# Kernel optimization log

Hardware: AMD Instinct MI355X
Metric: run time of the kernel (lower is better)

Reference implementation:

```python
import jax, jax.numpy as jnp
import numpy as np

N_NODES = 100000
N_EDGES = 1600000
N_GRAPHS = 512


def gcn_conv(x, src, dst, W, b, n_nodes):
    """PyG GCNConv: add self-loops, symmetric norm, linear, scatter-add, bias."""
    h = x @ W.T                                   # [N, out]
    ones = jnp.ones(src.shape[0], dtype=x.dtype)
    deg = jax.ops.segment_sum(ones, dst, num_segments=n_nodes)   # in-degree incl. self-loops
    dinv = jnp.where(deg > 0, jax.lax.rsqrt(deg), 0.0)
    norm = dinv[src] * dinv[dst]                  # [E+N]
    msg = h[src] * norm[:, None]                  # gather + scale
    out = jax.ops.segment_sum(msg, dst, num_segments=n_nodes)
    return out + b


def setup_inputs() -> dict:
    key = jax.random.key(0)
    ks = jax.random.split(key, 8)
    x = jax.random.normal(ks[0], (N_NODES, 2), dtype=jnp.float32)
    edge_index = jax.random.randint(ks[1], (2, N_EDGES), 0, N_NODES, dtype=jnp.int64)
    batch = jnp.sort(jax.random.randint(ks[2], (N_NODES,), 0, N_GRAPHS, dtype=jnp.int64))
    def glorot(k, shape):
        lim = jnp.sqrt(6.0 / (shape[0] + shape[1])).astype(jnp.float32)
        return jax.random.uniform(k, shape, jnp.float32, -lim, lim)
    return {
        "x": x, "edge_index": edge_index, "batch": batch,
        "W1": glorot(ks[3], (32, 2)),  "b1": jnp.zeros(32, jnp.float32),
        "W2": glorot(ks[4], (64, 32)), "b2": jnp.zeros(64, jnp.float32),
        "W3": glorot(ks[5], (32, 64)), "b3": jnp.zeros(32, jnp.float32),
        "Wfc": glorot(ks[6], (1, 32)), "bfc": jnp.zeros(1, jnp.float32),
    }


def reference(x, edge_index, batch, W1, b1, W2, b2, W3, b3, Wfc, bfc):
    n = x.shape[0]
    loop = jnp.arange(n, dtype=edge_index.dtype)
    src = jnp.concatenate([edge_index[0], loop])  # self-loops appended once
    dst = jnp.concatenate([edge_index[1], loop])

    h = jax.nn.relu(gcn_conv(x, src, dst, W1, b1, n))   # dropout = identity (eval)
    h = jax.nn.relu(gcn_conv(h, src, dst, W2, b2, n))
    h = jax.nn.relu(gcn_conv(h, src, dst, W3, b3, n))

    # global_mean_pool over graph ids
    sums = jax.ops.segment_sum(h, batch, num_segments=N_GRAPHS)
    cnts = jax.ops.segment_sum(jnp.ones((n,), h.dtype), batch, num_segments=N_GRAPHS)
    pooled = sums / jnp.maximum(cnts, 1.0)[:, None]     # [G, 32]
    return pooled @ Wfc.T + bfc                         # [G, 1]
```

## Files before the change

### kernel.cpp

```cpp
#include <hip/hip_runtime.h>
#include <hip/hip_fp16.h>


static constexpr int TPB = 256;
static constexpr int NB1 = 256;
static constexpr int NB_SCAN = 256;
static constexpr int P2CAP = 6144;

__global__ void p1_hist_kernel(const int* __restrict__ dst, int* __restrict__ hist,
                               int E, int chunk, int shift, int B) {
  __shared__ int h[1024];
  int b = blockIdx.x, t = threadIdx.x;
  for (int i = t; i < B; i += TPB) h[i] = 0;
  __syncthreads();
  int lo = b * chunk, hi = min(lo + chunk, E);
  for (int e = lo + t; e < hi; e += TPB) atomicAdd(&h[dst[e] >> shift], 1);
  __syncthreads();
  for (int i = t; i < B; i += TPB) hist[i * NB1 + b] = h[i];
}

__global__ void scan_partial_kernel(const int* __restrict__ a, int* __restrict__ bsum,
                                    int n, int seg) {
  int b = blockIdx.x, t = threadIdx.x;
  int lo = b * seg, hi = min(lo + seg, n);
  int acc = 0;
  for (int i = lo + t; i < hi; i += TPB) acc += a[i];
  __shared__ int red[TPB];
  red[t] = acc;
  __syncthreads();
  for (int st = TPB / 2; st > 0; st >>= 1) {
    if (t < st) red[t] += red[t + st];
    __syncthreads();
  }
  if (t == 0) bsum[b] = red[0];
}

__global__ void scan_blocks_kernel(int* __restrict__ bsum) {
  __shared__ int cs[NB_SCAN];
  int t = threadIdx.x;
  int v = bsum[t];
  cs[t] = v;
  __syncthreads();
  for (int off = 1; off < NB_SCAN; off <<= 1) {
    int u = (t >= off) ? cs[t - off] : 0;
    __syncthreads();
    cs[t] += u;
    __syncthreads();
  }
  bsum[t] = cs[t] - v;
}

__global__ void scan_emit_kernel(int* __restrict__ a, const int* __restrict__ bsum,
                                 int n, int seg) {
  int b = blockIdx.x, t = threadIdx.x;
  int lo = b * seg, hi = min(lo + seg, n);
  __shared__ int cs[TPB];
  __shared__ int s_run;
  if (t == 0) s_run = bsum[b];
  __syncthreads();
  for (int base = lo; base < hi; base += TPB) {
    int i = base + t;
    int v = (i < hi) ? a[i] : 0;
    cs[t] = v;
    __syncthreads();
    for (int off = 1; off < TPB; off <<= 1) {
      int u = (t >= off) ? cs[t - off] : 0;
      __syncthreads();
      cs[t] += u;
      __syncthreads();
    }
    if (i < hi) a[i] = s_run + cs[t] - v;
    __syncthreads();
    if (t == 0) s_run += cs[TPB - 1];
    __syncthreads();
  }
}

__global__ void p1_scatter_kernel(const int* __restrict__ src, const int* __restrict__ dst,
                                  const int* __restrict__ hist, unsigned int* __restrict__ epk,
                                  int E, int chunk, int shift, int srcbits, int B) {
  __shared__ int cur[1024];
  int b = blockIdx.x, t = threadIdx.x;
  for (int i = t; i < B; i += TPB) cur[i] = hist[i * NB1 + b];
  __syncthreads();
  int lo = b * chunk, hi = min(lo + chunk, E);
  int span1 = (1 << shift) - 1;
  for (int e = lo + t; e < hi; e += TPB) {
    int d = dst[e];
    int pos = atomicAdd(&cur[d >> shift], 1);
    epk[pos] = ((unsigned int)(d & span1) << srcbits) | (unsigned int)src[e];
  }
}

__global__ __launch_bounds__(TPB) void p2_sort_kernel(
    const unsigned int* __restrict__ epk, const int* __restrict__ hist,
    const float2* __restrict__ x2,
    int* __restrict__ rowptr, float* __restrict__ dinv, float2* __restrict__ u0,
    int* __restrict__ esrc, int N, int E, int shift, int srcbits, int B) {
  int bkt = blockIdx.x, t = threadIdx.x;
  int span = 1 << shift;
  unsigned int smask = (1u << srcbits) - 1u;
  int nb = bkt << shift;
  int bstart = hist[bkt * NB1];
  int bend = (bkt + 1 < B) ? hist[(bkt + 1) * NB1] : E;
  int bsize = bend - bstart;
  __shared__ int cnt[256];
  __shared__ int ex[256];
  __shared__ int lsrc[P2CAP];
  if (t < span) cnt[t] = 0;
  __syncthreads();
  for (int e = bstart + t; e < bend; e += TPB) atomicAdd(&cnt[epk[e] >> srcbits], 1);
  __syncthreads();
  int v = (t < span) ? cnt[t] : 0;
  ex[t] = v;
  __syncthreads();
  for (int off = 1; off < 256; off <<= 1) {
    int u = (t >= off) ? ex[t - off] : 0;
    __syncthreads();
    ex[t] += u;
    __syncthreads();
  }
  int excl = ex[t] - v;
  int node = nb + t;
  if (t < span && node < N) {
    rowptr[node] = bstart + excl;
    float dv = rsqrtf((float)v + 1.0f);
    dinv[node] = dv;
    float2 xv = x2[node];
    u0[node] = make_float2(xv.x * dv, xv.y * dv);
  }
  if (bkt == 0 && t == 0) rowptr[N] = E;
  __syncthreads();
  bool stage = (bsize <= P2CAP);
  if (t < span) cnt[t] = stage ? excl : bstart + excl;
  __syncthreads();
  for (int e = bstart + t; e < bend; e += TPB) {
    unsigned int p = epk[e];
    int pos = atomicAdd(&cnt[p >> srcbits], 1);
    if (stage) lsrc[pos] = (int)(p & smask);
    else esrc[pos] = (int)(p & smask);
  }
  __syncthreads();
  if (stage)
    for (int i = t; i < bsize; i += TPB) esrc[bstart + i] = lsrc[i];
}

__global__ void gptr_kernel(const int* __restrict__ batch, int* __restrict__ gstart, int n, int G) {
  int i = blockIdx.x * blockDim.x + threadIdx.x;
  if (i >= n) return;
  int b = batch[i];
  int bp = (i == 0) ? -1 : batch[i - 1];
  for (int g = bp + 1; g <= b; ++g) gstart[g] = i;
  if (i == n - 1)
    for (int g = b + 1; g <= G; ++g) gstart[g] = n;
}

__global__ void layer1_kernel(const float2* __restrict__ u0, const int* __restrict__ rowptr,
                              const int* __restrict__ esrc, const float* __restrict__ W1,
                              const float* __restrict__ b1, const float* __restrict__ dinv,
                              float* __restrict__ u1_32, __half* __restrict__ u1_16, int n) {
  int tid = blockIdx.x * blockDim.x + threadIdx.x;
  int i = tid >> 2, split = tid & 3;
  if (i >= n) return;
  float ax = 0.f, ay = 0.f;
  if (split == 0) {
    float2 s = u0[i];
    ax = s.x; ay = s.y;
  }
  int r0 = rowptr[i], r1 = rowptr[i + 1];
  for (int e = r0 + split; e < r1; e += 4) {
    float2 v = u0[esrc[e]];
    ax += v.x; ay += v.y;
  }
  ax += __shfl_xor(ax, 1, 64); ay += __shfl_xor(ay, 1, 64);
  ax += __shfl_xor(ax, 2, 64); ay += __shfl_xor(ay, 2, 64);
  float di = dinv[i];
  int f0 = split * 8;
  float o[8];
  union { float4 f4[1]; __half h[8]; } oh;
#pragma unroll
  for (int k = 0; k < 8; ++k) {
    int f = f0 + k;
    float hv = fmaxf(di * (W1[f * 2 + 0] * ax + W1[f * 2 + 1] * ay) + b1[f], 0.f);
    float uv = di * hv;
    o[k] = uv;
    oh.h[k] = __float2half(uv);
  }
  *(float4*)&u1_32[(size_t)i * 32 + f0] = make_float4(o[0], o[1], o[2], o[3]);
  *(float4*)&u1_32[(size_t)i * 32 + f0 + 4] = make_float4(o[4], o[5], o[6], o[7]);
  *(float4*)&u1_16[(size_t)i * 32 + f0] = oh.f4[0];
}

template <bool EPI>
__global__ void gather32_kernel(const float4* __restrict__ a32, const float4* __restrict__ a16,
                                const int* __restrict__ rowptr, const int* __restrict__ esrc,
                                const float* __restrict__ dinv, const float* __restrict__ b,
                                float4* __restrict__ out4, int n) {
  int tid = blockIdx.x * blockDim.x + threadIdx.x;
  int i = tid >> 4;
  int sub = tid & 15;
  int split = sub >> 2, q = sub & 3;
  if (i >= n) return;
  float acc[8] = {0.f, 0.f, 0.f, 0.f, 0.f, 0.f, 0.f, 0.f};
  if (split == 0) {
    float4 s0 = a32[(size_t)i * 8 + 2 * q];
    float4 s1 = a32[(size_t)i * 8 + 2 * q + 1];
    acc[0] = s0.x; acc[1] = s0.y; acc[2] = s0.z; acc[3] = s0.w;
    acc[4] = s1.x; acc[5] = s1.y; acc[6] = s1.z; acc[7] = s1.w;
  }
  int r0 = rowptr[i], r1 = rowptr[i + 1];
  for (int e = r0 + split; e < r1; e += 4) {
    int s = esrc[e];
    union { float4 f4; __half2 h2[4]; } u;
    u.f4 = a16[(size_t)s * 4 + q];
    float2 a0 = __half22float2(u.h2[0]);
    float2 a1 = __half22float2(u.h2[1]);
    float2 a2 = __half22float2(u.h2[2]);
    float2 a3 = __half22float2(u.h2[3]);
    acc[0] += a0.x; acc[1] += a0.y; acc[2] += a1.x; acc[3] += a1.y;
    acc[4] += a2.x; acc[5] += a2.y; acc[6] += a3.x; acc[7] += a3.y;
  }
#pragma unroll
  for (int k = 0; k < 8; ++k) acc[k] += __shfl_xor(acc[k], 4, 64);
#pragma unroll
  for (int k = 0; k < 8; ++k) acc[k] += __shfl_xor(acc[k], 8, 64);
  if (split != 0) return;
  float4 o0, o1;
  if (EPI) {
    float di = dinv[i];
    const float4 bv0 = ((const float4*)b)[2 * q];
    const float4 bv1 = ((const float4*)b)[2 * q + 1];
    o0.x = fmaxf(di * acc[0] + bv0.x, 0.f);
    o0.y = fmaxf(di * acc[1] + bv0.y, 0.f);
    o0.z = fmaxf(di * acc[2] + bv0.z, 0.f);
    o0.w = fmaxf(di * acc[3] + bv0.w, 0.f);
    o1.x = fmaxf(di * acc[4] + bv1.x, 0.f);
    o1.y = fmaxf(di * acc[5] + bv1.y, 0.f);
    o1.z = fmaxf(di * acc[6] + bv1.z, 0.f);
    o1.w = fmaxf(di * acc[7] + bv1.w, 0.f);
  } else {
    o0 = make_float4(acc[0], acc[1], acc[2], acc[3]);
    o1 = make_float4(acc[4], acc[5], acc[6], acc[7]);
  }
  out4[(size_t)i * 8 + 2 * q] = o0;
  out4[(size_t)i * 8 + 2 * q + 1] = o1;
}

__global__ __launch_bounds__(TPB) void t2t3_kernel(
    const float* __restrict__ U1, const float* __restrict__ W2, const float* __restrict__ b2,
    const float* __restrict__ W3, const float* __restrict__ dinv,
    float* __restrict__ g3_32, __half* __restrict__ g3_16, int n) {
  constexpr int SN = 136;
  __shared__ float U1l[32 * SN];
  __shared__ float h2l[64 * SN];
  __shared__ float W2l[32 * 68];
  __shared__ float W3l[64 * 36];
  __shared__ float dil[128];
  int t = threadIdx.x;
  int base = blockIdx.x * 128;
  for (int idx = t; idx < 2048; idx += TPB) {
    int k = idx >> 5, j = idx & 31;
    W2l[j * 68 + k] = W2[idx];
  }
  for (int idx = t; idx < 2048; idx += TPB) {
    int k = idx >> 6, j = idx & 63;
    W3l[j * 36 + k] = W3[idx];
  }
  if (t < 128) dil[t] = (base + t < n) ? dinv[base + t] : 0.f;
  for (int it = 0; it < 4; ++it) {
    int idx = it * 256 + t;
    int nl = idx >> 3, j0 = (idx & 7) * 4;
    int node = base + nl;
    float4 v = (node < n) ? ((const float4*)U1)[(size_t)node * 8 + (idx & 7)]
                          : make_float4(0.f, 0.f, 0.f, 0.f);
    U1l[(j0 + 0) * SN + nl] = v.x;
    U1l[(j0 + 1) * SN + nl] = v.y;
    U1l[(j0 + 2) * SN + nl] = v.z;
    U1l[(j0 + 3) * SN + nl] = v.w;
  }
  __syncthreads();
  {
    int a = t & 15, bb = t >> 4;
    int n0 = a * 8, k0 = bb * 4;
    float acc[4][8];
#pragma unroll
    for (int kk = 0; kk < 4; ++kk)
#pragma unroll
      for (int nn = 0; nn < 8; ++nn) acc[kk][nn] = 0.f;
#pragma unroll 8
    for (int j = 0; j < 32; ++j) {
      float4 ua = *(const float4*)&U1l[j * SN + n0];
      float4 ub = *(const float4*)&U1l[j * SN + n0 + 4];
      float4 w = *(const float4*)&W2l[j * 68 + k0];
      float un[8] = {ua.x, ua.y, ua.z, ua.w, ub.x, ub.y, ub.z, ub.w};
      float wk[4] = {w.x, w.y, w.z, w.w};
#pragma unroll
      for (int kk = 0; kk < 4; ++kk)
#pragma unroll
        for (int nn = 0; nn < 8; ++nn) acc[kk][nn] += un[nn] * wk[kk];
    }
    float4 bv = ((const float4*)b2)[bb];
    float bk[4] = {bv.x, bv.y, bv.z, bv.w};
#pragma unroll
    for (int kk = 0; kk < 4; ++kk) {
      float o[8];
#pragma unroll
      for (int nn = 0; nn < 8; ++nn)
        o[nn] = fmaxf(dil[n0 + nn] * acc[kk][nn] + bk[kk], 0.f);
      *(float4*)&h2l[(k0 + kk) * SN + n0] = make_float4(o[0], o[1], o[2], o[3]);
      *(float4*)&h2l[(k0 + kk) * SN + n0 + 4] = make_float4(o[4], o[5], o[6], o[7]);
    }
  }
  __syncthreads();
  {
    int a = t & 15, bb = t >> 4;
    int n0 = a * 8, k0 = bb * 2;
    float acc[2][8];
#pragma unroll
    for (int kk = 0; kk < 2; ++kk)
#pragma unroll
      for (int nn = 0; nn < 8; ++nn) acc[kk][nn] = 0.f;
#pragma unroll 8
    for (int j = 0; j < 64; ++j) {
      float4 ua = *(const float4*)&h2l[j * SN + n0];
      float4 ub = *(const float4*)&h2l[j * SN + n0 + 4];
      float w0 = W3l[j * 36 + k0];
      float w1 = W3l[j * 36 + k0 + 1];
      float un[8] = {ua.x, ua.y, ua.z, ua.w, ub.x, ub.y, ub.z, ub.w};
#pragma unroll
      for (int nn = 0; nn < 8; ++nn) {
        acc[0][nn] += un[nn] * w0;
        acc[1][nn] += un[nn] * w1;
      }
    }
#pragma unroll
    for (int nn = 0; nn < 8; ++nn) {
      int node = base + n0 + nn;
      if (node < n) {
        float di = dil[n0 + nn];
#pragma unroll
        for (int kk = 0; kk < 2; ++kk) {
          float gv = di * acc[kk][nn];
          g3_32[(size_t)node * 32 + k0 + kk] = gv;
          g3_16[(size_t)node * 32 + k0 + kk] = __float2half(gv);
        }
      }
    }
  }
}

__global__ void poolfc_kernel(const float* __restrict__ h3, const int* __restrict__ gstart,
                              const float* __restrict__ Wfc, const float* __restrict__ bfc,
                              float* __restrict__ out) {
  int gi = blockIdx.x;
  int s = gstart[gi], e = gstart[gi + 1];
  int t = threadIdx.x;
  int nl = t >> 5, f = t & 31;
  float acc = 0.f;
  for (int i = s + nl; i < e; i += 8) acc += h3[(size_t)i * 32 + f];
  __shared__ float red[256];
  red[t] = acc;
  __syncthreads();
  for (int st = 128; st >= 32; st >>= 1) {
    if (t < st) red[t] += red[t + st];
    __syncthreads();
  }
  if (t < 32) {
    float cnt = (float)(e - s);
    float v = (red[t] / fmaxf(cnt, 1.f)) * Wfc[t];
    for (int o = 16; o; o >>= 1) v += __shfl_down(v, o, 32);
    if (t == 0) out[gi] = v + bfc[0];
  }
}

extern "C" void kernel_launch(void* const* d_in, const int* in_sizes, int n_in,
                              void* d_out, int out_size, void* d_ws, size_t ws_size,
                              hipStream_t stream) {
  const float* x     = (const float*)d_in[0];
  const int*   ei    = (const int*)d_in[1];
  const int*   batch = (const int*)d_in[2];
  const float* W1    = (const float*)d_in[3];
  const float* b1    = (const float*)d_in[4];
  const float* W2    = (const float*)d_in[5];
  const float* b2    = (const float*)d_in[6];
  const float* W3    = (const float*)d_in[7];
  const float* b3    = (const float*)d_in[8];
  const float* Wfc   = (const float*)d_in[9];
  const float* bfc   = (const float*)d_in[10];
  float* out = (float*)d_out;

  const int N = in_sizes[0] / 2;
  const int E = in_sizes[1] / 2;
  const int G = out_size;
  const int* src = ei;
  const int* dst = ei + E;

  int shift = 7;
  while ((((N + (1 << shift) - 1) >> shift)) > 1024) ++shift;
  const int B = (N + (1 << shift) - 1) >> shift;
  const int srcbits = 32 - shift;
  const int chunkE = (E + NB1 - 1) / NB1;
  const int M = B * NB1;
  const int segM = (M + NB_SCAN - 1) / NB_SCAN;

  char* ws = (char*)d_ws;
  size_t off = 0;
  auto alloc = [&](size_t bytes) -> char* {
    char* p = ws + off;
    off += (bytes + 255) & ~(size_t)255;
    return p;
  };
  float*        dinv   = (float*)alloc((size_t)N * 4);
  int*          rowptr = (int*)alloc((size_t)(N + 1) * 4);
  int*          esrc   = (int*)alloc((size_t)E * 4);
  int*          gstart = (int*)alloc((size_t)(G + 1) * 4);
  int*          hist   = (int*)alloc((size_t)M * 4);
  int*          bsum   = (int*)alloc((size_t)NB_SCAN * 4);
  unsigned int* epk    = (unsigned int*)alloc((size_t)E * 4);
  float2*       u0     = (float2*)alloc((size_t)N * 8);
  float*        u1_32  = (float*)alloc((size_t)N * 32 * 4);
  __half*       u1_16  = (__half*)alloc((size_t)N * 32 * 2);
  float*        U1     = (float*)alloc((size_t)N * 32 * 4);
  float*        g3_32  = (float*)alloc((size_t)N * 32 * 4);
  __half*       g3_16  = (__half*)alloc((size_t)N * 32 * 2);
  float*        hA     = (float*)alloc((size_t)N * 32 * 4);

  p1_hist_kernel<<<NB1, TPB, 0, stream>>>(dst, hist, E, chunkE, shift, B);
  scan_partial_kernel<<<NB_SCAN, TPB, 0, stream>>>(hist, bsum, M, segM);
  scan_blocks_kernel<<<1, NB_SCAN, 0, stream>>>(bsum);
  scan_emit_kernel<<<NB_SCAN, TPB, 0, stream>>>(hist, bsum, M, segM);
  p1_scatter_kernel<<<NB1, TPB, 0, stream>>>(src, dst, hist, epk, E, chunkE, shift, srcbits, B);
  p2_sort_kernel<<<B, TPB, 0, stream>>>(epk, hist, (const float2*)x, rowptr, dinv, u0, esrc,
                                        N, E, shift, srcbits, B);
  gptr_kernel<<<(N + TPB - 1) / TPB, TPB, 0, stream>>>(batch, gstart, N, G);

  layer1_kernel<<<((size_t)N * 4 + TPB - 1) / TPB, TPB, 0, stream>>>(
      u0, rowptr, esrc, W1, b1, dinv, u1_32, u1_16, N);

  gather32_kernel<false><<<((size_t)N * 16 + TPB - 1) / TPB, TPB, 0, stream>>>(
      (const float4*)u1_32, (const float4*)u1_16, rowptr, esrc, dinv, b2, (float4*)U1, N);
  t2t3_kernel<<<(N + 127) / 128, TPB, 0, stream>>>(U1, W2, b2, W3, dinv, g3_32, g3_16, N);

  gather32_kernel<true><<<((size_t)N * 16 + TPB - 1) / TPB, TPB, 0, stream>>>(
      (const float4*)g3_32, (const float4*)g3_16, rowptr, esrc, dinv, b3, (float4*)hA, N);

  poolfc_kernel<<<G, 256, 0, stream>>>(hA, gstart, Wfc, bfc, out);
}
```

Measured before the change: 248.1 us.

## Drop fp32 feature copies, fold block scan into emit, prefetch edge indices

Removes the fp32 copies of the layer-1 and layer-3 features. The self-loop term in the gathers is now read from the fp16 buffer, which cuts global writes of about 12.8 MB per buffer and the matching reads. The separate single-block scan kernel is replaced by each emit block reducing the partial sums of the blocks before it, which saves one launch. Edge-loop index loads are software-pipelined one step ahead. In exchange, the self-loop contribution now carries fp16 rounding error.

```diff
diff --git a/kernel.cpp b/kernel.cpp
--- a/kernel.cpp
+++ b/kernel.cpp
@@ -35,28 +35,19 @@
   if (t == 0) bsum[b] = red[0];
 }
 
-__global__ void scan_blocks_kernel(int* __restrict__ bsum) {
-  __shared__ int cs[NB_SCAN];
-  int t = threadIdx.x;
-  int v = bsum[t];
-  cs[t] = v;
-  __syncthreads();
-  for (int off = 1; off < NB_SCAN; off <<= 1) {
-    int u = (t >= off) ? cs[t - off] : 0;
-    __syncthreads();
-    cs[t] += u;
-    __syncthreads();
-  }
-  bsum[t] = cs[t] - v;
-}
-
 __global__ void scan_emit_kernel(int* __restrict__ a, const int* __restrict__ bsum,
                                  int n, int seg) {
   int b = blockIdx.x, t = threadIdx.x;
   int lo = b * seg, hi = min(lo + seg, n);
   __shared__ int cs[TPB];
   __shared__ int s_run;
-  if (t == 0) s_run = bsum[b];
+  cs[t] = (t < b) ? bsum[t] : 0;
+  __syncthreads();
+  for (int st = TPB / 2; st > 0; st >>= 1) {
+    if (t < st) cs[t] += cs[t + st];
+    __syncthreads();
+  }
+  if (t == 0) s_run = cs[0];
   __syncthreads();
   for (int base = lo; base < hi; base += TPB) {
     int i = base + t;
@@ -158,7 +149,7 @@
 __global__ void layer1_kernel(const float2* __restrict__ u0, const int* __restrict__ rowptr,
                               const int* __restrict__ esrc, const float* __restrict__ W1,
                               const float* __restrict__ b1, const float* __restrict__ dinv,
-                              float* __restrict__ u1_32, __half* __restrict__ u1_16, int n) {
+                              __half* __restrict__ u1_16, int n) {
   int tid = blockIdx.x * blockDim.x + threadIdx.x;
   int i = tid >> 2, split = tid & 3;
   if (i >= n) return;
@@ -168,31 +159,34 @@
     ax = s.x; ay = s.y;
   }
   int r0 = rowptr[i], r1 = rowptr[i + 1];
-  for (int e = r0 + split; e < r1; e += 4) {
-    float2 v = u0[esrc[e]];
+  int e = r0 + split;
+  if (e < r1) {
+    int snext = esrc[e];
+    for (e += 4; e < r1; e += 4) {
+      int scur = snext;
+      snext = esrc[e];
+      float2 v = u0[scur];
+      ax += v.x; ay += v.y;
+    }
+    float2 v = u0[snext];
     ax += v.x; ay += v.y;
   }
   ax += __shfl_xor(ax, 1, 64); ay += __shfl_xor(ay, 1, 64);
   ax += __shfl_xor(ax, 2, 64); ay += __shfl_xor(ay, 2, 64);
   float di = dinv[i];
   int f0 = split * 8;
-  float o[8];
   union { float4 f4[1]; __half h[8]; } oh;
 #pragma unroll
   for (int k = 0; k < 8; ++k) {
     int f = f0 + k;
     float hv = fmaxf(di * (W1[f * 2 + 0] * ax + W1[f * 2 + 1] * ay) + b1[f], 0.f);
-    float uv = di * hv;
-    o[k] = uv;
-    oh.h[k] = __float2half(uv);
-  }
-  *(float4*)&u1_32[(size_t)i * 32 + f0] = make_float4(o[0], o[1], o[2], o[3]);
-  *(float4*)&u1_32[(size_t)i * 32 + f0 + 4] = make_float4(o[4], o[5], o[6], o[7]);
+    oh.h[k] = __float2half(di * hv);
+  }
   *(float4*)&u1_16[(size_t)i * 32 + f0] = oh.f4[0];
 }
 
 template <bool EPI>
-__global__ void gather32_kernel(const float4* __restrict__ a32, const float4* __restrict__ a16,
+__global__ void gather32_kernel(const float4* __restrict__ a16,
                                 const int* __restrict__ rowptr, const int* __restrict__ esrc,
                                 const float* __restrict__ dinv, const float* __restrict__ b,
                                 float4* __restrict__ out4, int n) {
@@ -202,15 +196,7 @@
   int split = sub >> 2, q = sub & 3;
   if (i >= n) return;
   float acc[8] = {0.f, 0.f, 0.f, 0.f, 0.f, 0.f, 0.f, 0.f};
-  if (split == 0) {
-    float4 s0 = a32[(size_t)i * 8 + 2 * q];
-    float4 s1 = a32[(size_t)i * 8 + 2 * q + 1];
-    acc[0] = s0.x; acc[1] = s0.y; acc[2] = s0.z; acc[3] = s0.w;
-    acc[4] = s1.x; acc[5] = s1.y; acc[6] = s1.z; acc[7] = s1.w;
-  }
-  int r0 = rowptr[i], r1 = rowptr[i + 1];
-  for (int e = r0 + split; e < r1; e += 4) {
-    int s = esrc[e];
+  auto addrow = [&](int s) {
     union { float4 f4; __half2 h2[4]; } u;
     u.f4 = a16[(size_t)s * 4 + q];
     float2 a0 = __half22float2(u.h2[0]);
@@ -219,6 +205,18 @@
     float2 a3 = __half22float2(u.h2[3]);
     acc[0] += a0.x; acc[1] += a0.y; acc[2] += a1.x; acc[3] += a1.y;
     acc[4] += a2.x; acc[5] += a2.y; acc[6] += a3.x; acc[7] += a3.y;
+  };
+  if (split == 0) addrow(i);
+  int r0 = rowptr[i], r1 = rowptr[i + 1];
+  int e = r0 + split;
+  if (e < r1) {
+    int snext = esrc[e];
+    for (e += 4; e < r1; e += 4) {
+      int scur = snext;
+      snext = esrc[e];
+      addrow(scur);
+    }
+    addrow(snext);
   }
 #pragma unroll
   for (int k = 0; k < 8; ++k) acc[k] += __shfl_xor(acc[k], 4, 64);
@@ -249,7 +247,7 @@
 __global__ __launch_bounds__(TPB) void t2t3_kernel(
     const float* __restrict__ U1, const float* __restrict__ W2, const float* __restrict__ b2,
     const float* __restrict__ W3, const float* __restrict__ dinv,
-    float* __restrict__ g3_32, __half* __restrict__ g3_16, int n) {
+    __half* __restrict__ g3_16, int n) {
   constexpr int SN = 136;
   __shared__ float U1l[32 * SN];
   __shared__ float h2l[64 * SN];
@@ -339,11 +337,8 @@
       if (node < n) {
         float di = dil[n0 + nn];
 #pragma unroll
-        for (int kk = 0; kk < 2; ++kk) {
-          float gv = di * acc[kk][nn];
-          g3_32[(size_t)node * 32 + k0 + kk] = gv;
-          g3_16[(size_t)node * 32 + k0 + kk] = __float2half(gv);
-        }
+        for (int kk = 0; kk < 2; ++kk)
+          g3_16[(size_t)node * 32 + k0 + kk] = __float2half(di * acc[kk][nn]);
       }
     }
   }
@@ -418,16 +413,13 @@
   int*          bsum   = (int*)alloc((size_t)NB_SCAN * 4);
   unsigned int* epk    = (unsigned int*)alloc((size_t)E * 4);
   float2*       u0     = (float2*)alloc((size_t)N * 8);
-  float*        u1_32  = (float*)alloc((size_t)N * 32 * 4);
   __half*       u1_16  = (__half*)alloc((size_t)N * 32 * 2);
   float*        U1     = (float*)alloc((size_t)N * 32 * 4);
-  float*        g3_32  = (float*)alloc((size_t)N * 32 * 4);
   __half*       g3_16  = (__half*)alloc((size_t)N * 32 * 2);
   float*        hA     = (float*)alloc((size_t)N * 32 * 4);
 
   p1_hist_kernel<<<NB1, TPB, 0, stream>>>(dst, hist, E, chunkE, shift, B);
   scan_partial_kernel<<<NB_SCAN, TPB, 0, stream>>>(hist, bsum, M, segM);
-  scan_blocks_kernel<<<1, NB_SCAN, 0, stream>>>(bsum);
   scan_emit_kernel<<<NB_SCAN, TPB, 0, stream>>>(hist, bsum, M, segM);
   p1_scatter_kernel<<<NB1, TPB, 0, stream>>>(src, dst, hist, epk, E, chunkE, shift, srcbits, B);
   p2_sort_kernel<<<B, TPB, 0, stream>>>(epk, hist, (const float2*)x, rowptr, dinv, u0, esrc,
@@ -435,14 +427,14 @@
   gptr_kernel<<<(N + TPB - 1) / TPB, TPB, 0, stream>>>(batch, gstart, N, G);
 
   layer1_kernel<<<((size_t)N * 4 + TPB - 1) / TPB, TPB, 0, stream>>>(
-      u0, rowptr, esrc, W1, b1, dinv, u1_32, u1_16, N);
+      u0, rowptr, esrc, W1, b1, dinv, u1_16, N);
 
   gather32_kernel<false><<<((size_t)N * 16 + TPB - 1) / TPB, TPB, 0, stream>>>(
-      (const float4*)u1_32, (const float4*)u1_16, rowptr, esrc, dinv, b2, (float4*)U1, N);
-  t2t3_kernel<<<(N + 127) / 128, TPB, 0, stream>>>(U1, W2, b2, W3, dinv, g3_32, g3_16, N);
+      (const float4*)u1_16, rowptr, esrc, dinv, b2, (float4*)U1, N);
+  t2t3_kernel<<<(N + 127) / 128, TPB, 0, stream>>>(U1, W2, b2, W3, dinv, g3_16, N);
 
   gather32_kernel<true><<<((size_t)N * 16 + TPB - 1) / TPB, TPB, 0, stream>>>(
-      (const float4*)g3_32, (const float4*)g3_16, rowptr, esrc, dinv, b3, (float4*)hA, N);
+      (const float4*)g3_16, rowptr, esrc, dinv, b3, (float4*)hA, N);
 
   poolfc_kernel<<<G, 256, 0, stream>>>(hA, gstart, Wfc, bfc, out);
 }
```

New measurement: 228.7 us. 1.09x faster.
